# Kernel tuning notes

Measured on AMD Instinct MI355X. Metric: run time of the kernel, lower is better.

The kernel has to match this reference:

```python
import jax, jax.numpy as jnp
import numpy as np

B, A, N, L = 4, 16, 8, 512
DE, DH, H, C = 256, 64, 8, 1.0
DHEAD = DE // H
LN_EPS = 1e-5

def _layernorm(x, w, b):
    mu = jnp.mean(x, axis=-1, keepdims=True)
    var = jnp.mean((x - mu) ** 2, axis=-1, keepdims=True)
    return (x - mu) / jnp.sqrt(var + LN_EPS) * w + b

def _logmap0(x, c):
    sc = jnp.sqrt(c)
    n = jnp.maximum(jnp.linalg.norm(x, axis=-1, keepdims=True), 1e-15)
    u = jnp.minimum(sc * n, 1.0 - 1e-5)  # stay inside artanh domain
    return jnp.arctanh(u) * x / (sc * n)

def _expmap0(u, c):
    sc = jnp.sqrt(c)
    n = jnp.maximum(jnp.linalg.norm(u, axis=-1, keepdims=True), 1e-15)
    return jnp.tanh(sc * n) * u / (sc * n)

def setup_inputs() -> dict:
    key = jax.random.key(0)
    ks = jax.random.split(key, 5)
    curr_rho = jax.random.normal(ks[0], (B, A, DE), jnp.float32)
    demo_rho = jax.random.normal(ks[1], (B, N, L, A, DE), jnp.float32)
    demo_hyp = jax.random.normal(ks[2], (B, N, L, DH), jnp.float32)
    # project hyperbolic points inside the unit Poincare ball
    demo_hyp = demo_hyp / (1.0 + jnp.linalg.norm(demo_hyp, axis=-1, keepdims=True)) * 0.9
    demo_mask = jnp.ones((B, N, L), jnp.int32)
    Wq = jax.random.normal(ks[3], (DE, DE), jnp.float32) / np.sqrt(DE)
    Wk = jax.random.normal(ks[4], (DE, DE), jnp.float32) / np.sqrt(DE)
    return {"curr_rho": curr_rho, "demo_rho": demo_rho, "demo_hyp": demo_hyp,
            "demo_mask": demo_mask, "Wq": Wq, "Wk": Wk,
            "ln_q_w": jnp.ones((DE,), jnp.float32), "ln_q_b": jnp.zeros((DE,), jnp.float32),
            "ln_k_w": jnp.ones((DE,), jnp.float32), "ln_k_b": jnp.zeros((DE,), jnp.float32)}

def reference(curr_rho, demo_rho, demo_hyp, demo_mask, Wq, Wk, ln_q_w, ln_q_b, ln_k_w, ln_k_b):
    # queries: [B,H,A,dh]
    q = (_layernorm(curr_rho, ln_q_w, ln_q_b) @ Wq.T).reshape(B, A, H, DHEAD).transpose(0, 2, 1, 3)
    # keys: [B,N,L,A,H,dh]; the original gather over agents with arange(A) is identity,
    # so scores align query agent a with key agent a directly.
    k = (_layernorm(demo_rho, ln_k_w, ln_k_b) @ Wk.T).reshape(B, N, L, A, H, DHEAD)
    scores = jnp.einsum('bhad,bnlahd->bhanl', q, k) / np.sqrt(DHEAD)  # [B,H,A,N,L]
    dm = demo_mask[:, None, None, :, :]
    scores = jnp.where(dm == 0, -jnp.inf, scores)
    attn_flat = jax.nn.softmax(scores.reshape(B, H, A, N * L), axis=-1)
    # Poincare weighted mean in tangent space at origin
    vals_tan0 = _logmap0(demo_hyp.reshape(B, N * L, DH), C)          # [B,NL,dh_h]
    m_h = jnp.einsum('bhax,bxd->bhad', attn_flat, vals_tan0)          # [B,H,A,d_h]
    y_h_tan0 = _logmap0(_expmap0(m_h, C), C)
    curr_hyp = _expmap0(jnp.mean(y_h_tan0, axis=1), C)                # [B,A,d_h]
    max_rad = 1.0 / np.sqrt(C) - 1e-5
    norm = jnp.maximum(jnp.linalg.norm(curr_hyp, axis=-1, keepdims=True), 1e-6)
    curr_hyp = curr_hyp * jnp.minimum(max_rad / norm, 1.0)
    curr_hyp = jnp.mean(curr_hyp, axis=1)                             # [B,d_h] (as in source)
    return curr_hyp, attn_flat.reshape(B, H, A, N, L)
```

## Files before the change

### kernel.cpp

```cpp
#include <hip/hip_runtime.h>
#include <math.h>

#define LN_EPS_ 1e-5f
#define INV_SQRT_DHEAD 0.17677669529663687f


__device__ __forceinline__ float waveReduceSum(float v) {
    #pragma unroll
    for (int m = 32; m > 0; m >>= 1) v += __shfl_xor(v, m, 64);
    return v;
}
__device__ __forceinline__ float waveReduceMax(float v) {
    #pragma unroll
    for (int m = 32; m > 0; m >>= 1) v = fmaxf(v, __shfl_xor(v, m, 64));
    return v;
}

__global__ __launch_bounds__(256) void k_prep(
    const float* __restrict__ curr_rho, const float* __restrict__ Wq,
    const float* __restrict__ Wk, const float* __restrict__ lnqw,
    const float* __restrict__ lnqb, const float* __restrict__ lnkw,
    const float* __restrict__ lnkb,
    float* __restrict__ g, float* __restrict__ s0, float* __restrict__ s2)
{
    __shared__ float xs[256];
    __shared__ float qs[256];
    __shared__ float red[8];
    const int t = threadIdx.x;
    const int w = t >> 6;
    const int ba = blockIdx.x;
    const float x = curr_rho[(size_t)ba * 256 + t];

    float sm = waveReduceSum(x);
    if ((t & 63) == 0) red[w] = sm;
    __syncthreads();
    const float mu = (red[0] + red[1] + red[2] + red[3]) * (1.0f / 256.0f);
    __syncthreads();
    const float dx = x - mu;
    float sq = waveReduceSum(dx * dx);
    if ((t & 63) == 0) red[w] = sq;
    __syncthreads();
    const float var = (red[0] + red[1] + red[2] + red[3]) * (1.0f / 256.0f);
    const float rstd = 1.0f / sqrtf(var + LN_EPS_);
    __syncthreads();
    xs[t] = dx * rstd * lnqw[t] + lnqb[t];
    __syncthreads();

    {
        const float4* wq4 = (const float4*)(Wq + (size_t)t * 256);
        float acc = 0.f;
        #pragma unroll 8
        for (int e4 = 0; e4 < 64; ++e4) {
            float4 wv = wq4[e4];
            acc += xs[e4*4+0]*wv.x + xs[e4*4+1]*wv.y + xs[e4*4+2]*wv.z + xs[e4*4+3]*wv.w;
        }
        qs[t] = acc;
    }
    __syncthreads();

    for (int h = 0; h < 8; ++h) {
        float qk = 0.f;
        #pragma unroll 8
        for (int dh = 0; dh < 32; ++dh)
            qk += qs[h*32+dh] * Wk[(size_t)(h*32+dh)*256 + t];
        const float gv = lnkw[t] * qk;
        const float b2 = lnkb[t] * qk;
        g[((size_t)ba * 8 + h) * 256 + t] = gv;
        float sg = waveReduceSum(gv);
        float sb = waveReduceSum(b2);
        if ((t & 63) == 0) { red[w] = sg; red[4 + w] = sb; }
        __syncthreads();
        if (t == 0) {
            s0[ba*8+h] = red[0] + red[1] + red[2] + red[3];
            s2[ba*8+h] = red[4] + red[5] + red[6] + red[7];
        }
        __syncthreads();
    }
}

__global__ __launch_bounds__(256) void k_vals(
    const float* __restrict__ demo_hyp, float* __restrict__ vals)
{
    const int t = threadIdx.x;
    const size_t idx = (size_t)blockIdx.x * 256 + t;
    const float x = demo_hyp[idx];
    const float ss = waveReduceSum(x * x);
    const float nrm = sqrtf(ss);
    const float n = fmaxf(nrm, 1e-15f);
    const float u = fminf(n, 1.0f - 1e-5f);
    const float f = atanhf(u) / n;
    vals[idx] = x * f;
}

__global__ __launch_bounds__(256) void k_scores(
    const float* __restrict__ demo_rho, const int* __restrict__ demo_mask,
    const float* __restrict__ g, const float* __restrict__ s0,
    const float* __restrict__ s2, float* __restrict__ attn)
{
    __shared__ float sbuf[8][132];
    const int t = threadIdx.x;
    const int gid = blockIdx.x;
    const int lc = gid & 3;
    const int n  = (gid >> 2) & 7;
    const int a  = (gid >> 5) & 15;
    const int b  = gid >> 9;
    const int c  = t & 31;
    const int r  = t >> 5;

    float gr[8][8];
    {
        const float* gb = g + ((size_t)(b*16 + a) * 8) * 256 + c * 8;
        #pragma unroll
        for (int h = 0; h < 8; ++h) {
            float4 ga = *(const float4*)(gb + h * 256);
            float4 gc = *(const float4*)(gb + h * 256 + 4);
            gr[h][0]=ga.x; gr[h][1]=ga.y; gr[h][2]=ga.z; gr[h][3]=ga.w;
            gr[h][4]=gc.x; gr[h][5]=gc.y; gr[h][6]=gc.z; gr[h][7]=gc.w;
        }
    }
    const float s0v = s0[(b*16 + a) * 8 + (c & 7)];
    const float s2v = s2[(b*16 + a) * 8 + (c & 7)];
    const int* mrow = demo_mask + (b*8 + n) * 512 + lc * 128;

    const float* xbase = demo_rho +
        ((size_t)((b*8 + n) * 512 + lc * 128) * 16 + a) * 256 + c * 8;

    #pragma unroll 2
    for (int p = 0; p < 16; ++p) {
        const float* xp = xbase + (size_t)(p * 8 + r) * 4096;
        float4 xa = *(const float4*)(xp);
        float4 xb = *(const float4*)(xp + 4);
        float xv[8] = {xa.x, xa.y, xa.z, xa.w, xb.x, xb.y, xb.z, xb.w};

        float v[10];
        #pragma unroll
        for (int h = 0; h < 8; ++h) {
            float acc = 0.f;
            #pragma unroll
            for (int j = 0; j < 8; ++j) acc += xv[j] * gr[h][j];
            v[h] = acc;
        }
        float sm = 0.f, sq = 0.f;
        #pragma unroll
        for (int j = 0; j < 8; ++j) { sm += xv[j]; sq += xv[j] * xv[j]; }
        v[8] = sm; v[9] = sq;

        const int lb0 = c & 1, lb1 = c & 2, lb2 = c & 4, lb3 = c & 8;
        float a0 = lb0 ? v[1] : v[0]; float q0 = lb0 ? v[0] : v[1];
        a0 += __shfl_xor(q0, 1, 32);
        float a1 = lb0 ? v[3] : v[2]; float q1 = lb0 ? v[2] : v[3];
        a1 += __shfl_xor(q1, 1, 32);
        float a2 = lb0 ? v[5] : v[4]; float q2 = lb0 ? v[4] : v[5];
        a2 += __shfl_xor(q2, 1, 32);
        float a3 = lb0 ? v[7] : v[6]; float q3 = lb0 ? v[6] : v[7];
        a3 += __shfl_xor(q3, 1, 32);
        float a4 = lb0 ? v[9] : v[8]; float q4 = lb0 ? v[8] : v[9];
        a4 += __shfl_xor(q4, 1, 32);
        float w0 = lb1 ? a1 : a0; float r0 = lb1 ? a0 : a1;
        w0 += __shfl_xor(r0, 2, 32);
        float w1 = lb1 ? a3 : a2; float r1 = lb1 ? a2 : a3;
        w1 += __shfl_xor(r1, 2, 32);
        float w2 = a4 + __shfl_xor(a4, 2, 32);
        float x0 = lb2 ? w1 : w0; float r2 = lb2 ? w0 : w1;
        x0 += __shfl_xor(r2, 4, 32);
        float x1 = w2 + __shfl_xor(w2, 4, 32);
        float y = lb3 ? x1 : x0; float r3 = lb3 ? x0 : x1;
        y += __shfl_xor(r3, 8, 32);
        y += __shfl_xor(y, 16, 32);
        const float smv = __shfl(y, 8, 32);
        const float sqv = __shfl(y, 9, 32);

        if (c < 8) {
            const float mu   = smv * (1.0f / 256.0f);
            const float var  = sqv * (1.0f / 256.0f) - mu * mu;
            const float rstd = 1.0f / sqrtf(var + LN_EPS_);
            float sc = (rstd * (y - mu * s0v) + s2v) * INV_SQRT_DHEAD;
            const int lidx = p * 8 + r;
            if (mrow[lidx] == 0) sc = -INFINITY;
            sbuf[c][lidx] = sc;
        }
    }
    __syncthreads();
    {
        const int h = t >> 5;
        const float* rowp = &sbuf[h][0];
        float4 vout = *(const float4*)(rowp + c * 4);
        const size_t off = (size_t)((b*8 + h) * 16 + a) * 4096 + n * 512 + lc * 128 + c * 4;
        *(float4*)(attn + off) = vout;
    }
}

__global__ __launch_bounds__(512) void k_softmax_mh(
    float* __restrict__ attn, const float* __restrict__ vals,
    float* __restrict__ mh)
{
    __shared__ float p0[4096];
    __shared__ float p1[4096];
    __shared__ float red[2][4];
    __shared__ float mpart[2][8][64];
    const int t = threadIdx.x;
    const int half = t >> 8;
    const int tt = t & 255;
    const int w = tt >> 6;
    const int row0 = blockIdx.x * 2;
    const int row = row0 + half;
    const int b = row0 >> 7;

    float* dst = attn + (size_t)row * 4096;
    float* pl = half ? p1 : p0;

    float lmax = -INFINITY;
    float4 v4[4];
    #pragma unroll
    for (int k = 0; k < 4; ++k) {
        float4 vv = ((const float4*)dst)[k * 256 + tt];
        v4[k] = vv;
        lmax = fmaxf(lmax, fmaxf(fmaxf(vv.x, vv.y), fmaxf(vv.z, vv.w)));
    }
    lmax = waveReduceMax(lmax);
    if ((tt & 63) == 0) red[half][w] = lmax;
    __syncthreads();
    const float mx = fmaxf(fmaxf(red[half][0], red[half][1]),
                           fmaxf(red[half][2], red[half][3]));
    __syncthreads();
    float lsum = 0.f;
    #pragma unroll
    for (int k = 0; k < 4; ++k) {
        float4 vv = v4[k];
        vv.x = __expf(vv.x - mx); vv.y = __expf(vv.y - mx);
        vv.z = __expf(vv.z - mx); vv.w = __expf(vv.w - mx);
        v4[k] = vv;
        lsum += vv.x + vv.y + vv.z + vv.w;
    }
    lsum = waveReduceSum(lsum);
    if ((tt & 63) == 0) red[half][w] = lsum;
    __syncthreads();
    const float inv = 1.0f / (red[half][0] + red[half][1] +
                              red[half][2] + red[half][3]);
    #pragma unroll
    for (int k = 0; k < 4; ++k) {
        float4 vv = v4[k];
        vv.x *= inv; vv.y *= inv; vv.z *= inv; vv.w *= inv;
        ((float4*)pl)[k * 256 + tt] = vv;
        ((float4*)dst)[k * 256 + tt] = vv;
    }
    __syncthreads();

    const int ch = t >> 6, d = t & 63;
    const float* vb = vals + (size_t)b * 262144 + d;
    float acc0a = 0.f, acc0b = 0.f, acc1a = 0.f, acc1b = 0.f;
    const int x0 = ch * 512;
    #pragma unroll 16
    for (int x = x0; x < x0 + 512; x += 2) {
        const float va = vb[(size_t)x * 64];
        const float vc = vb[(size_t)(x + 1) * 64];
        acc0a += p0[x] * va;     acc0b += p0[x + 1] * vc;
        acc1a += p1[x] * va;     acc1b += p1[x + 1] * vc;
    }
    mpart[0][ch][d] = acc0a + acc0b;
    mpart[1][ch][d] = acc1a + acc1b;
    __syncthreads();
    if (t < 128) {
        const int rr = t >> 6, dd = t & 63;
        float s = 0.f;
        #pragma unroll
        for (int cc = 0; cc < 8; ++cc) s += mpart[rr][cc][dd];
        mh[(size_t)(row0 + rr) * 64 + dd] = s;
    }
}

__global__ __launch_bounds__(1024) void k_final(
    const float* __restrict__ mh, float* __restrict__ out)
{
    __shared__ float contrib[16][64];
    const int t = threadIdx.x;
    const int a = t >> 6, d = t & 63;
    const int b = blockIdx.x;
    float accY = 0.f;
    #pragma unroll
    for (int h = 0; h < 8; ++h) {
        const float m = mh[(size_t)((b*8 + h) * 16 + a) * 64 + d];
        const float ss = waveReduceSum(m * m);
        const float nm = sqrtf(ss);
        const float n1 = fmaxf(nm, 1e-15f);
        const float t1 = tanhf(n1);
        const float e  = t1 * m / n1;
        const float ne = t1 * nm / n1;
        const float n2 = fmaxf(ne, 1e-15f);
        const float u  = fminf(n2, 1.0f - 1e-5f);
        accY += atanhf(u) * e / n2;
    }
    const float ym = accY * 0.125f;
    const float ssy = waveReduceSum(ym * ym);
    const float nmy = sqrtf(ssy);
    const float n3 = fmaxf(nmy, 1e-15f);
    const float t3 = tanhf(n3);
    const float chv = t3 * ym / n3;
    const float nch = t3 * nmy / n3;
    const float nrm = fmaxf(nch, 1e-6f);
    const float sc = fminf((1.0f - 1e-5f) / nrm, 1.0f);
    contrib[a][d] = chv * sc;
    __syncthreads();
    if (t < 64) {
        float s = 0.f;
        #pragma unroll
        for (int a2 = 0; a2 < 16; ++a2) s += contrib[a2][t];
        out[b * 64 + t] = s * (1.0f / 16.0f);
    }
}

extern "C" void kernel_launch(void* const* d_in, const int* in_sizes, int n_in,
                              void* d_out, int out_size, void* d_ws, size_t ws_size,
                              hipStream_t stream) {
    const float* curr_rho  = (const float*)d_in[0];
    const float* demo_rho  = (const float*)d_in[1];
    const float* demo_hyp  = (const float*)d_in[2];
    const int*   demo_mask = (const int*)d_in[3];
    const float* Wq   = (const float*)d_in[4];
    const float* Wk   = (const float*)d_in[5];
    const float* lnqw = (const float*)d_in[6];
    const float* lnqb = (const float*)d_in[7];
    const float* lnkw = (const float*)d_in[8];
    const float* lnkb = (const float*)d_in[9];

    float* out  = (float*)d_out;
    float* attn = out + 256;

    float* ws   = (float*)d_ws;
    float* g    = ws;
    float* s0   = ws + 131072;
    float* s2   = ws + 131584;
    float* vals = ws + 132096;
    float* mh   = ws + 1180672;

    hipLaunchKernelGGL(k_prep, dim3(64), dim3(256), 0, stream,
                       curr_rho, Wq, Wk, lnqw, lnqb, lnkw, lnkb, g, s0, s2);
    hipLaunchKernelGGL(k_vals, dim3(4096), dim3(256), 0, stream, demo_hyp, vals);
    hipLaunchKernelGGL(k_scores, dim3(2048), dim3(256), 0, stream,
                       demo_rho, demo_mask, g, s0, s2, attn);
    hipLaunchKernelGGL(k_softmax_mh, dim3(256), dim3(512), 0, stream, attn, vals, mh);
    hipLaunchKernelGGL(k_final, dim3(4), dim3(1024), 0, stream, mh, out);
}
```

Before: 445.9 us.

## Merge prep and vals kernels, split prep per head, remap softmax blocks to XCDs

Fuses the small prep kernel and the logmap vals kernel into one launch. Prep work now runs one block per (batch-agent, head) instead of looping over eight heads in each of 64 blocks. This gives more parallelism but recomputes the layernorm and the Wq projection eight times. The softmax kernel's block index is permuted so that rows sharing a batch land on the same XCD, which is meant to improve L2 locality for the vals reads. The main cost targeted is launch overhead and the serial head loop; the whole pipeline is dominated by the large scores kernel over demo_rho, so the gain is small either way.

```diff
diff --git a/kernel.cpp b/kernel.cpp
--- a/kernel.cpp
+++ b/kernel.cpp
@@ -16,19 +16,34 @@
     return v;
 }
 
-__global__ __launch_bounds__(256) void k_prep(
+__global__ __launch_bounds__(256) void k_prep_vals(
     const float* __restrict__ curr_rho, const float* __restrict__ Wq,
     const float* __restrict__ Wk, const float* __restrict__ lnqw,
     const float* __restrict__ lnqb, const float* __restrict__ lnkw,
-    const float* __restrict__ lnkb,
-    float* __restrict__ g, float* __restrict__ s0, float* __restrict__ s2)
+    const float* __restrict__ lnkb, const float* __restrict__ demo_hyp,
+    float* __restrict__ g, float* __restrict__ s0, float* __restrict__ s2,
+    float* __restrict__ vals)
 {
     __shared__ float xs[256];
     __shared__ float qs[256];
     __shared__ float red[8];
     const int t = threadIdx.x;
+    const int bid = blockIdx.x;
+
+    if (bid >= 512) {
+        const size_t idx = (size_t)(bid - 512) * 256 + t;
+        const float x = demo_hyp[idx];
+        const float ss = waveReduceSum(x * x);
+        const float nrm = sqrtf(ss);
+        const float n = fmaxf(nrm, 1e-15f);
+        const float u = fminf(n, 1.0f - 1e-5f);
+        vals[idx] = x * (atanhf(u) / n);
+        return;
+    }
+
     const int w = t >> 6;
-    const int ba = blockIdx.x;
+    const int ba = bid >> 3;
+    const int h  = bid & 7;
     const float x = curr_rho[(size_t)ba * 256 + t];
 
     float sm = waveReduceSum(x);
@@ -58,38 +73,21 @@
     }
     __syncthreads();
 
-    for (int h = 0; h < 8; ++h) {
-        float qk = 0.f;
-        #pragma unroll 8
-        for (int dh = 0; dh < 32; ++dh)
-            qk += qs[h*32+dh] * Wk[(size_t)(h*32+dh)*256 + t];
-        const float gv = lnkw[t] * qk;
-        const float b2 = lnkb[t] * qk;
-        g[((size_t)ba * 8 + h) * 256 + t] = gv;
-        float sg = waveReduceSum(gv);
-        float sb = waveReduceSum(b2);
-        if ((t & 63) == 0) { red[w] = sg; red[4 + w] = sb; }
-        __syncthreads();
-        if (t == 0) {
-            s0[ba*8+h] = red[0] + red[1] + red[2] + red[3];
-            s2[ba*8+h] = red[4] + red[5] + red[6] + red[7];
-        }
-        __syncthreads();
-    }
-}
-
-__global__ __launch_bounds__(256) void k_vals(
-    const float* __restrict__ demo_hyp, float* __restrict__ vals)
-{
-    const int t = threadIdx.x;
-    const size_t idx = (size_t)blockIdx.x * 256 + t;
-    const float x = demo_hyp[idx];
-    const float ss = waveReduceSum(x * x);
-    const float nrm = sqrtf(ss);
-    const float n = fmaxf(nrm, 1e-15f);
-    const float u = fminf(n, 1.0f - 1e-5f);
-    const float f = atanhf(u) / n;
-    vals[idx] = x * f;
+    float qk = 0.f;
+    #pragma unroll 8
+    for (int dh = 0; dh < 32; ++dh)
+        qk += qs[h*32+dh] * Wk[(size_t)(h*32+dh)*256 + t];
+    const float gv = lnkw[t] * qk;
+    const float b2 = lnkb[t] * qk;
+    g[((size_t)ba * 8 + h) * 256 + t] = gv;
+    float sg = waveReduceSum(gv);
+    float sb = waveReduceSum(b2);
+    if ((t & 63) == 0) { red[w] = sg; red[4 + w] = sb; }
+    __syncthreads();
+    if (t == 0) {
+        s0[ba*8+h] = red[0] + red[1] + red[2] + red[3];
+        s2[ba*8+h] = red[4] + red[5] + red[6] + red[7];
+    }
 }
 
 __global__ __launch_bounds__(256) void k_scores(
@@ -202,7 +200,10 @@
     const int half = t >> 8;
     const int tt = t & 255;
     const int w = tt >> 6;
-    const int row0 = blockIdx.x * 2;
+    const int j = blockIdx.x;
+    const int xcd = j & 7, slot = j >> 3;
+    const int rp = (xcd >> 1) * 64 + (xcd & 1) * 32 + slot;
+    const int row0 = rp * 2;
     const int row = row0 + half;
     const int b = row0 >> 7;
 
@@ -333,9 +334,9 @@
     float* vals = ws + 132096;
     float* mh   = ws + 1180672;
 
-    hipLaunchKernelGGL(k_prep, dim3(64), dim3(256), 0, stream,
-                       curr_rho, Wq, Wk, lnqw, lnqb, lnkw, lnkb, g, s0, s2);
-    hipLaunchKernelGGL(k_vals, dim3(4096), dim3(256), 0, stream, demo_hyp, vals);
+    hipLaunchKernelGGL(k_prep_vals, dim3(4608), dim3(256), 0, stream,
+                       curr_rho, Wq, Wk, lnqw, lnqb, lnkw, lnkb, demo_hyp,
+                       g, s0, s2, vals);
     hipLaunchKernelGGL(k_scores, dim3(2048), dim3(256), 0, stream,
                        demo_rho, demo_mask, g, s0, s2, attn);
     hipLaunchKernelGGL(k_softmax_mh, dim3(256), dim3(512), 0, stream, attn, vals, mh);
```

Result: faster. 429.2 us (-3.7%).
